# Optimization experiments

Measured on AMD Instinct MI355X. Metric: run time of the kernel, lower is better.

Reference implementation:

```python
import jax, jax.numpy as jnp
import numpy as np

B, T, F, M = 32, 256, 512, 4   # batch, pred_len (=d_model=state_size), feature_dim (=mamba seq), time-mark feats
N = F - M                      # number of variates in x_enc
T2 = 2 * T
EPS = 1e-5


def setup_inputs() -> dict:
    key = jax.random.key(0)
    it = iter(jax.random.split(key, 32))
    def nrm(*s):
        return jax.random.normal(next(it), s, jnp.float32) * 0.02
    inp = {
        "x_enc": jax.random.normal(next(it), (B, T, N), jnp.float32),
        "x_mark_enc": jax.random.normal(next(it), (B, T, M), jnp.float32),
        "x_dec": jnp.zeros((1, 1, 1), jnp.float32),
        "x_mark_dec": jnp.zeros((1, 1, 1), jnp.float32),
        # 3 structurally identical MambaBlocks -> stack params on leading dim 3
        "norm_w": jnp.ones((3, T), jnp.float32),
        "inp_W": nrm(3, T, T2), "inp_b": jnp.zeros((3, T2), jnp.float32),
        "conv_W": nrm(3, F, F, 3), "conv_b": jnp.zeros((3, F), jnp.float32),
        "convlin_W": nrm(3, T2, T2), "convlin_b": jnp.zeros((3, T2), jnp.float32),
        "fc1_W": nrm(3, T2, T2), "fc1_b": jnp.zeros((3, T2), jnp.float32),
        "fc2_W": nrm(3, T2, T), "fc2_b": jnp.zeros((3, T), jnp.float32),
        "fc3_W": nrm(3, T2, T), "fc3_b": jnp.zeros((3, T), jnp.float32),
        "D_W": nrm(3, T, T2), "D_b": jnp.zeros((3, T2), jnp.float32),
        "out_W": nrm(3, T2, T), "out_b": jnp.ones((3, T), jnp.float32),  # out_proj.bias init to 1.0
        "proj_W": nrm(T, T), "proj_b": jnp.zeros((T,), jnp.float32),
    }
    return inp


def _rmsnorm(x, w):
    return x * jax.lax.rsqrt(jnp.mean(x * x, -1, keepdims=True) + EPS) * w


def _conv1d(x, W, b):
    # x: [B, C, L], W: [C_out, C_in, 3], padding=1
    y = jax.lax.conv_general_dilated(x, W, (1,), [(1, 1)], dimension_numbers=("NCH", "OIH", "NCH"))
    return y + b[None, :, None]


def _s6(x, fc1W, fc1b, fc2W, fc2b, fc3W, fc3b):
    # h is zero-initialized each call, so dA=exp(delta*A) multiplies zeros and
    # y = einsum('bln,bldn->bld', C, x[...,None]*dB) = delta * x * <C,B>_n
    Bmat = x @ fc2W + fc2b                         # [B, L, n]
    Cmat = x @ fc3W + fc3b                         # [B, L, n]
    delta = jax.nn.softplus(x @ fc1W + fc1b)       # [B, L, d]
    cb = jnp.einsum("bln,bln->bl", Cmat, Bmat)   # contraction over state dim
    return delta * x * cb[:, :, None]


def _block(x, i, p):
    xn = _rmsnorm(x, p["norm_w"][i])
    xp = xn @ p["inp_W"][i] + p["inp_b"][i]                      # [B, F, 2T]
    xc = jax.nn.silu(_conv1d(xp, p["conv_W"][i], p["conv_b"][i]))
    xco = xc @ p["convlin_W"][i] + p["convlin_b"][i]
    xssm = _s6(xco, p["fc1_W"][i], p["fc1_b"][i], p["fc2_W"][i], p["fc2_b"][i], p["fc3_W"][i], p["fc3_b"][i])
    xres = jax.nn.silu(xn @ p["D_W"][i] + p["D_b"][i])
    return (jax.nn.silu(xssm) * xres) @ p["out_W"][i] + p["out_b"][i]


def _forward(x_enc, x_mark_enc, p):
    means = jax.lax.stop_gradient(jnp.mean(x_enc, 1, keepdims=True))  # detached in torch
    xe = x_enc - means
    stdev = jnp.sqrt(jnp.var(xe, axis=1, keepdims=True) + 1e-5)       # NOT detached in torch
    xe = xe / stdev
    x = jnp.concatenate([xe, x_mark_enc], axis=2).transpose(0, 2, 1)  # [B, F, T]
    for i in range(3):
        x = _block(x, i, p)
    dec = (x @ p["proj_W"] + p["proj_b"]).transpose(0, 2, 1)          # [B, T, F]
    return dec[:, :, :N] * stdev + means                              # pred_len == T


def reference(x_enc, x_mark_enc, x_dec, x_mark_dec, norm_w, inp_W, inp_b, conv_W, conv_b, convlin_W, convlin_b, fc1_W, fc1_b, fc2_W, fc2_b, fc3_W, fc3_b, D_W, D_b, out_W, out_b, proj_W, proj_b):
    p = dict(norm_w=norm_w, inp_W=inp_W, inp_b=inp_b, conv_W=conv_W, conv_b=conv_b, convlin_W=convlin_W, convlin_b=convlin_b, fc1_W=fc1_W, fc1_b=fc1_b, fc2_W=fc2_W, fc2_b=fc2_b, fc3_W=fc3_W, fc3_b=fc3_b, D_W=D_W, D_b=D_b, out_W=out_W, out_b=out_b, proj_W=proj_W, proj_b=proj_b)
    return _forward(x_enc, x_mark_enc, p)
```

## Files before the change

### kernel.cpp

```cpp
#include <hip/hip_runtime.h>
#include <hip/hip_bf16.h>
#include <math.h>

typedef __hip_bfloat16 bf16;
typedef short short8 __attribute__((ext_vector_type(8)));
typedef short short4v __attribute__((ext_vector_type(4)));
typedef float floatx4 __attribute__((ext_vector_type(4)));

constexpr int CB_ = 32;
constexpr int CT = 256;
constexpr int CF = 512;
constexpr int CN = 508;
constexpr int CM = 4;
constexpr int CT2 = 512;
constexpr int MROWS = CB_ * CF;
constexpr int PADL = 528;

__device__ __forceinline__ float b2f(bf16 v) { return __bfloat162float(v); }
__device__ __forceinline__ bf16 f2b(float v) { return __float2bfloat16(v); }
__device__ __forceinline__ short f2s(float v) {
    bf16 t = __float2bfloat16(v);
    return __builtin_bit_cast(short, t);
}
__device__ __forceinline__ float silu_f(float x) { return x / (1.0f + __expf(-x)); }
__device__ __forceinline__ float softplus_f(float x) {
    return fmaxf(x, 0.0f) + __logf(1.0f + __expf(-fabsf(x)));
}

__device__ __forceinline__ void gl_lds16(const bf16* g, short* l) {
    __builtin_amdgcn_global_load_lds(
        (const __attribute__((address_space(1))) unsigned int*)(g),
        (__attribute__((address_space(3))) unsigned int*)(l), 16, 0, 0);
}


constexpr int CONVN = 3 * 3 * 512 * 512;
constexpr int MTILES = 3520;
struct P8 { const float* s[8]; bf16* d[8]; };
__global__ __launch_bounds__(256) void prepack_all_kernel(P8 p, const float* __restrict__ nw,
                                                          const float* __restrict__ convW,
                                                          bf16* __restrict__ convD,
                                                          bf16* __restrict__ xpT,
                                                          float* __restrict__ CBv) {
    int bid = blockIdx.x;
    if (bid >= MTILES) {
        int idx = (bid - MTILES) * 256 + threadIdx.x;
        if (idx < CONVN) {
            int ci = idx & 511;
            int co = (idx >> 9) & 511;
            int it = idx >> 18;
            int tap = it % 3, ib = it / 3;
            convD[idx] = f2b(convW[(((size_t)(ib * 512 + co)) * 512 + ci) * 3 + tap]);
        } else if (idx < CONVN + 32768) {
            int j = idx - CONVN;
            int ci = j & 511;
            int w = (j >> 9) & 1;
            int b = j >> 10;
            xpT[((size_t)b * PADL + (w ? 513 : 0)) * 512 + ci] = f2b(0.0f);
        } else if (idx < CONVN + 32768 + MROWS) {
            CBv[idx - CONVN - 32768] = 0.0f;
        }
        return;
    }
    const int Ks[8]   = {256, 256, 512, 512, 512, 512, 512, 256};
    const int Ns[8]   = {512, 512, 512, 256, 256, 512, 256, 256};
    const int zs[8]   = {3, 3, 3, 3, 3, 3, 3, 1};
    const int dstr[8] = {262144, 262144, 524288, 524288, 524288, 262144, 131072, 65536};
    const int rml[8]  = {1, 1, 1, 2, 2, 1, 1, 1};
    const int rad[8]  = {0, 0, 0, 0, 1, 0, 0, 0};
    int m = 0, acc = 0;
    for (m = 0; m < 8; m++) {
        int c = (Ns[m] >> 5) * (Ks[m] >> 5) * zs[m];
        if (bid < acc + c) break;
        acc += c;
    }
    int lid = bid - acc;
    int K = Ks[m], N = Ns[m];
    int tx = N >> 5, ty = K >> 5;
    int z = lid / (tx * ty), rem = lid % (tx * ty);
    int k0 = (rem / tx) * 32, n0 = (rem % tx) * 32;
    const float* s = p.s[m] + (size_t)z * K * N;
    bf16* d = p.d[m] + (size_t)z * dstr[m];
    int mul = rml[m], add = rad[m];
    bool fold = (m <= 1);
    __shared__ float Ts[32][33];
    for (int e = threadIdx.x; e < 1024; e += 256) {
        int r = e >> 5, c = e & 31;
        float v = s[(size_t)(k0 + r) * N + n0 + c];
        if (fold) v *= nw[z * 256 + k0 + r];
        Ts[r][c] = v;
    }
    __syncthreads();
    for (int e = threadIdx.x; e < 1024; e += 256) {
        int r = e >> 5, c = e & 31;
        d[(size_t)((n0 + r) * mul + add) * K + k0 + c] = f2b(Ts[c][r]);
    }
}

__global__ __launch_bounds__(256) void buildx_kernel(
    const float* __restrict__ xe, const float* __restrict__ xm,
    float* __restrict__ means, float* __restrict__ stdev,
    bf16* __restrict__ X0, float* __restrict__ SCL) {
    __shared__ float L[256][65];
    __shared__ float red_s[4][64], red_q[4][64];
    __shared__ float stat_m[64], stat_i[64];
    int blk = blockIdx.x;
    int b = blk >> 3, f0 = (blk & 7) * 64;
    int tid = threadIdx.x;
    int j = tid & 63, tq = tid >> 6;
    int f = f0 + j;
    float ps = 0.f, pq = 0.f;
    const float* xep = xe + (size_t)b * CT * CN + f;
    const float* xmp = xm + (size_t)b * CT * CM + (f - CN);
    #pragma unroll 4
    for (int tt = 0; tt < 64; tt++) {
        int t = tq * 64 + tt;
        float v = (f < CN) ? xep[(size_t)t * CN] : xmp[(size_t)t * CM];
        L[t][j] = v;
        ps += v;
        pq += v * v;
    }
    red_s[tq][j] = ps;
    red_q[tq][j] = pq;
    __syncthreads();
    if (tid < 64) {
        int ff = f0 + tid;
        float s = red_s[0][tid] + red_s[1][tid] + red_s[2][tid] + red_s[3][tid];
        float q = red_q[0][tid] + red_q[1][tid] + red_q[2][tid] + red_q[3][tid];
        float mean, isd, msq;
        if (ff < CN) {
            mean = s * (1.0f / 256.0f);
            float var = fmaxf(q * (1.0f / 256.0f) - mean * mean, 0.0f);
            float sd = sqrtf(var + 1e-5f);
            isd = 1.0f / sd;
            means[b * CN + ff] = mean;
            stdev[b * CN + ff] = sd;
            msq = var / (var + 1e-5f);
        } else {
            mean = 0.0f;
            isd = 1.0f;
            msq = q * (1.0f / 256.0f);
        }
        stat_m[tid] = mean;
        stat_i[tid] = isd;
        SCL[b * 512 + ff] = rsqrtf(msq + 1e-5f);
    }
    __syncthreads();
    bf16* outp = X0 + ((size_t)(b * 512 + f0)) * 256;
    int t = tid;
    #pragma unroll 4
    for (int fp = 0; fp < 64; fp++) {
        float val = (L[t][fp] - stat_m[fp]) * stat_i[fp];
        outp[(size_t)fp * 256 + t] = f2b(val);
    }
}

template <int MODE>
__global__ __launch_bounds__(256) void mgemm_kernel(const bf16* __restrict__ A,
                                                    const bf16* __restrict__ Wt,
                                                    const float* __restrict__ b1,
                                                    const float* __restrict__ b2,
                                                    const float* __restrict__ SCL,
                                                    bf16* __restrict__ o1,
                                                    bf16* __restrict__ o2,
                                                    int K, int Ncols) {
    __shared__ __align__(16) short As[128 * 64];
    __shared__ __align__(16) short Bs[128 * 64];
    const int tid = threadIdx.x;
    const int lane = tid & 63;
    const int wave = tid >> 6;
    const int m0 = blockIdx.x * 128, n0 = blockIdx.y * 128;

    const int srow0 = wave * 32;
    const int lrow8 = lane >> 3;
    const int lcolS = (((lane & 7) ^ lrow8) << 3);

    const bf16* aPc[4];
    const bf16* bPc[4];
    short* aLc[4];
    short* bLc[4];
    #pragma unroll
    for (int c = 0; c < 4; c++) {
        aPc[c] = A + (size_t)(m0 + srow0 + c * 8 + lrow8) * K + lcolS;
        bPc[c] = Wt + (size_t)(n0 + srow0 + c * 8 + lrow8) * K + lcolS;
        aLc[c] = &As[(srow0 + c * 8) * 64];
        bLc[c] = &Bs[(srow0 + c * 8) * 64];
    }

    const int wm = (wave & 1) * 64, wn = (wave >> 1) * 64;
    const int fr = lane & 15, quad = lane >> 4;
    const int fr7 = fr & 7;

    floatx4 acc[4][4];
    #pragma unroll
    for (int i = 0; i < 4; i++)
        #pragma unroll
        for (int j = 0; j < 4; j++) acc[i][j] = (floatx4){0.f, 0.f, 0.f, 0.f};

    for (int k0 = 0; k0 < K; k0 += 64) {
        #pragma unroll
        for (int c = 0; c < 4; c++) {
            gl_lds16(aPc[c] + k0, aLc[c]);
            gl_lds16(bPc[c] + k0, bLc[c]);
        }
        __syncthreads();
        #pragma unroll
        for (int s = 0; s < 2; s++) {
            const int co = (((s * 4 + quad) ^ fr7) << 3);
            short8 af[4], bfv[4];
            #pragma unroll
            for (int i = 0; i < 4; i++) af[i] = *(const short8*)&As[(wm + i * 16 + fr) * 64 + co];
            #pragma unroll
            for (int j = 0; j < 4; j++) bfv[j] = *(const short8*)&Bs[(wn + j * 16 + fr) * 64 + co];
            #pragma unroll
            for (int i = 0; i < 4; i++)
                #pragma unroll
                for (int j = 0; j < 4; j++)
                    acc[i][j] = __builtin_amdgcn_mfma_f32_16x16x32_bf16(af[i], bfv[j], acc[i][j], 0, 0, 0);
        }
        __syncthreads();
    }

    if (MODE == 0) {
        #pragma unroll
        for (int j = 0; j < 4; j++) {
            int n = n0 + wn + j * 16 + fr;
            float bv = b1[n];
            #pragma unroll
            for (int i = 0; i < 4; i++) {
                int mb = m0 + wm + i * 16 + quad * 4;
                #pragma unroll
                for (int r = 0; r < 4; r++)
                    o1[(size_t)(mb + r) * Ncols + n] = f2b(acc[i][j][r] + bv);
            }
        }
    } else {
        if (n0 + wn < 512) {
            int b = (m0 + wm) >> 9;
            #pragma unroll
            for (int i = 0; i < 4; i++) {
                int mb = m0 + wm + i * 16 + quad * 4;
                float sclr[4];
                #pragma unroll
                for (int r = 0; r < 4; r++) sclr[r] = SCL[mb + r];
                #pragma unroll
                for (int j = 0; j < 4; j++) {
                    int n = n0 + wn + j * 16 + fr;
                    float bv = b1[n];
                    bf16* dst = o1 + ((size_t)b * PADL + n + 1) * 512;
                    int ci = mb & 511;
                    short4v pk;
                    #pragma unroll
                    for (int r = 0; r < 4; r++) pk[r] = f2s(acc[i][j][r] * sclr[r] + bv);
                    *(short4v*)(dst + ci) = pk;
                }
            }
        } else {
            #pragma unroll
            for (int i = 0; i < 4; i++) {
                int mb = m0 + wm + i * 16 + quad * 4;
                float sclr[4];
                #pragma unroll
                for (int r = 0; r < 4; r++) sclr[r] = SCL[mb + r];
                #pragma unroll
                for (int j = 0; j < 4; j++) {
                    int n = n0 + wn + j * 16 + fr;
                    float bv = b2[n - 512];
                    #pragma unroll
                    for (int r = 0; r < 4; r++)
                        o2[(size_t)(mb + r) * 512 + (n - 512)] =
                            f2b(silu_f(acc[i][j][r] * sclr[r] + bv));
                }
            }
        }
    }
}

template <int EPI>
__global__ __launch_bounds__(256) void g64_kernel(const bf16* __restrict__ A,
                                                  const bf16* __restrict__ Wt,
                                                  int K,
                                                  const float* __restrict__ b1,
                                                  const float* __restrict__ b2,
                                                  const float* __restrict__ CBin,
                                                  const bf16* __restrict__ Xres,
                                                  float* __restrict__ CBout,
                                                  bf16* __restrict__ o1,
                                                  int Ncols,
                                                  const float* __restrict__ means,
                                                  const float* __restrict__ stdev,
                                                  float* __restrict__ outf) {
    __shared__ __align__(16) short As[128 * 64];
    __shared__ __align__(16) short Bs[64 * 64];
    const int tid = threadIdx.x;
    const int lane = tid & 63;
    const int wave = tid >> 6;
    const int m0 = blockIdx.x * 128, n0 = blockIdx.y * 64;

    const int lrow8 = lane >> 3;
    const int lcolS = (((lane & 7) ^ lrow8) << 3);
    const int wm = (wave & 1) * 64, wn = (wave >> 1) * 32;
    const int fr = lane & 15, quad = lane >> 4;
    const int fr7 = fr & 7;

    floatx4 acc[4][2];
    #pragma unroll
    for (int i = 0; i < 4; i++)
        #pragma unroll
        for (int j = 0; j < 2; j++) acc[i][j] = (floatx4){0.f, 0.f, 0.f, 0.f};

    for (int k0 = 0; k0 < K; k0 += 64) {
        for (int ca = wave; ca < 16; ca += 4)
            gl_lds16(A + (size_t)(m0 + ca * 8 + lrow8) * K + k0 + lcolS, &As[ca * 512]);
        for (int cb = wave; cb < 8; cb += 4)
            gl_lds16(Wt + (size_t)(n0 + cb * 8 + lrow8) * K + k0 + lcolS, &Bs[cb * 512]);
        __syncthreads();
        #pragma unroll
        for (int s = 0; s < 2; s++) {
            const int co = (((s * 4 + quad) ^ fr7) << 3);
            short8 af[4], bfv[2];
            #pragma unroll
            for (int i = 0; i < 4; i++) af[i] = *(const short8*)&As[(wm + i * 16 + fr) * 64 + co];
            #pragma unroll
            for (int j = 0; j < 2; j++) bfv[j] = *(const short8*)&Bs[(wn + j * 16 + fr) * 64 + co];
            #pragma unroll
            for (int i = 0; i < 4; i++)
                #pragma unroll
                for (int j = 0; j < 2; j++)
                    acc[i][j] = __builtin_amdgcn_mfma_f32_16x16x32_bf16(af[i], bfv[j], acc[i][j], 0, 0, 0);
        }
        __syncthreads();
    }

    if (EPI == 0) {
        #pragma unroll
        for (int j = 0; j < 2; j++) {
            int n = n0 + wn + j * 16 + fr;
            float bv = b1[n];
            #pragma unroll
            for (int i = 0; i < 4; i++) {
                int mb = m0 + wm + i * 16 + quad * 4;
                #pragma unroll
                for (int r = 0; r < 4; r++)
                    o1[(size_t)(mb + r) * Ncols + n] = f2b(acc[i][j][r] + bv);
            }
        }
    } else if (EPI == 1) {
        float bv[2];
        #pragma unroll
        for (int j = 0; j < 2; j++) {
            int nn = n0 + wn + j * 16 + fr;
            int c = nn >> 1;
            bv[j] = (fr & 1) ? b2[c] : b1[c];
        }
        #pragma unroll
        for (int i = 0; i < 4; i++) {
            #pragma unroll
            for (int r = 0; r < 4; r++) {
                float s = 0.f;
                #pragma unroll
                for (int j = 0; j < 2; j++) {
                    float v = acc[i][j][r] + bv[j];
                    s += v * __shfl_xor(v, 1);
                }
                s += __shfl_xor(s, 2);
                s += __shfl_xor(s, 4);
                s += __shfl_xor(s, 8);
                if (fr == 0)
                    atomicAdd(&CBout[m0 + wm + i * 16 + quad * 4 + r], s * 0.5f);
            }
        }
    } else if (EPI == 2) {
        #pragma unroll
        for (int i = 0; i < 4; i++) {
            int mb = m0 + wm + i * 16 + quad * 4;
            float cbr[4];
            #pragma unroll
            for (int r = 0; r < 4; r++) cbr[r] = CBin[mb + r];
            #pragma unroll
            for (int j = 0; j < 2; j++) {
                int n = n0 + wn + j * 16 + fr;
                float bv = b1[n];
                #pragma unroll
                for (int r = 0; r < 4; r++) {
                    size_t off = (size_t)(mb + r) * 512 + n;
                    float delta = softplus_f(acc[i][j][r] + bv);
                    float xssm = delta * b2f(A[off]) * cbr[r];
                    o1[off] = f2b(silu_f(xssm) * b2f(Xres[off]));
                }
            }
        }
    } else {
        #pragma unroll
        for (int j = 0; j < 2; j++) {
            int t = n0 + wn + j * 16 + fr;
            float bv = b1[t];
            #pragma unroll
            for (int i = 0; i < 4; i++) {
                int mb = m0 + wm + i * 16 + quad * 4;
                int b = mb >> 9;
                int nv = mb & 511;
                if (nv < CN) {
                    floatx4 o;
                    #pragma unroll
                    for (int r = 0; r < 4; r++) {
                        int sn = b * CN + nv + r;
                        o[r] = (acc[i][j][r] + bv) * stdev[sn] + means[sn];
                    }
                    *(floatx4*)(outf + ((size_t)(b * CT + t)) * CN + nv) = o;
                }
            }
        }
    }
}

__global__ __launch_bounds__(256) void conv_mfma_kernel(const bf16* __restrict__ Wc,
                                                        const bf16* __restrict__ xpT,
                                                        const float* __restrict__ bias,
                                                        bf16* __restrict__ Out,
                                                        float* __restrict__ CBvZ) {
    __shared__ __align__(16) short As[3 * 64 * 64];
    __shared__ __align__(16) short Bs[72 * 64];
    const int tid = threadIdx.x;
    const int lane = tid & 63;
    const int wave = tid >> 6;
    int bx = blockIdx.x;
    if (bx < 128 && tid < 128) CBvZ[bx * 128 + tid] = 0.0f;
    int b = bx >> 6, rem = bx & 63;
    int mt = rem >> 3, nt = rem & 7;
    const int m0 = mt * 64, n0 = nt * 64;
    const bf16* xb = xpT + (size_t)b * PADL * 512;

    const int lrow8 = lane >> 3;
    const int lcolS = (((lane & 7) ^ lrow8) << 3);
    const int wm = (wave & 1) * 32, wn = (wave >> 1) * 32;
    const int fr = lane & 15, quad = lane >> 4;
    const int fr7 = fr & 7;

    floatx4 acc[2][2];
    #pragma unroll
    for (int i = 0; i < 2; i++)
        #pragma unroll
        for (int j = 0; j < 2; j++) acc[i][j] = (floatx4){0.f, 0.f, 0.f, 0.f};

    for (int k0 = 0; k0 < 512; k0 += 64) {
        for (int ga = wave; ga < 24; ga += 4) {
            int tap = ga >> 3, rg = ga & 7;
            gl_lds16(Wc + (size_t)tap * 262144 + (size_t)(m0 + rg * 8 + lrow8) * 512 + k0 + lcolS,
                     &As[tap * 4096 + rg * 512]);
        }
        for (int gb = wave; gb < 9; gb += 4) {
            gl_lds16(xb + (size_t)(n0 + gb * 8 + lrow8) * 512 + k0 + lcolS, &Bs[gb * 512]);
        }
        __syncthreads();
        #pragma unroll
        for (int s = 0; s < 2; s++) {
            const int sq = s * 4 + quad;
            #pragma unroll
            for (int tap = 0; tap < 3; tap++) {
                const int coA = ((sq ^ fr7) << 3);
                const int coB = ((sq ^ ((fr + tap) & 7)) << 3);
                short8 af[2], bfv[2];
                #pragma unroll
                for (int i = 0; i < 2; i++)
                    af[i] = *(const short8*)&As[tap * 4096 + (wm + i * 16 + fr) * 64 + coA];
                #pragma unroll
                for (int j = 0; j < 2; j++)
                    bfv[j] = *(const short8*)&Bs[(wn + j * 16 + fr + tap) * 64 + coB];
                #pragma unroll
                for (int i = 0; i < 2; i++)
                    #pragma unroll
                    for (int j = 0; j < 2; j++)
                        acc[i][j] = __builtin_amdgcn_mfma_f32_16x16x32_bf16(af[i], bfv[j], acc[i][j], 0, 0, 0);
            }
        }
        __syncthreads();
    }
    bf16* ob = Out + (size_t)b * CF * CT2;
    #pragma unroll
    for (int i = 0; i < 2; i++) {
        int mb = m0 + wm + i * 16 + quad * 4;
        #pragma unroll
        for (int r = 0; r < 4; r++) {
            float bv = bias[mb + r];
            #pragma unroll
            for (int j = 0; j < 2; j++) {
                int n = n0 + wn + j * 16 + fr;
                ob[(size_t)(mb + r) * CT2 + n] = f2b(silu_f(acc[i][j][r] + bv));
            }
        }
    }
}

__global__ __launch_bounds__(256) void gemm_scl_kernel(const bf16* __restrict__ A,
                                                       const bf16* __restrict__ Wt,
                                                       const float* __restrict__ bias,
                                                       bf16* __restrict__ Xo,
                                                       float* __restrict__ SCL) {
    __shared__ __align__(16) short As[32 * 64];
    __shared__ __align__(16) short Bs[256 * 64];
    __shared__ float red[4][32];
    const int tid = threadIdx.x;
    const int lane = tid & 63;
    const int wave = tid >> 6;
    const int m0 = blockIdx.x * 32;

    const int lrow8 = lane >> 3;
    const int lcolS = (((lane & 7) ^ lrow8) << 3);
    const int wn = wave * 64;
    const int fr = lane & 15, quad = lane >> 4;
    const int fr7 = fr & 7;

    floatx4 acc[2][4];
    #pragma unroll
    for (int i = 0; i < 2; i++)
        #pragma unroll
        for (int j = 0; j < 4; j++) acc[i][j] = (floatx4){0.f, 0.f, 0.f, 0.f};

    for (int k0 = 0; k0 < 512; k0 += 64) {
        for (int c = wave; c < 4; c += 4)
            gl_lds16(A + (size_t)(m0 + c * 8 + lrow8) * 512 + k0 + lcolS, &As[c * 512]);
        for (int c = wave; c < 32; c += 4)
            gl_lds16(Wt + (size_t)(c * 8 + lrow8) * 512 + k0 + lcolS, &Bs[c * 512]);
        __syncthreads();
        #pragma unroll
        for (int s = 0; s < 2; s++) {
            const int co = (((s * 4 + quad) ^ fr7) << 3);
            short8 af[2], bfv[4];
            #pragma unroll
            for (int i = 0; i < 2; i++) af[i] = *(const short8*)&As[(i * 16 + fr) * 64 + co];
            #pragma unroll
            for (int j = 0; j < 4; j++) bfv[j] = *(const short8*)&Bs[(wn + j * 16 + fr) * 64 + co];
            #pragma unroll
            for (int i = 0; i < 2; i++)
                #pragma unroll
                for (int j = 0; j < 4; j++)
                    acc[i][j] = __builtin_amdgcn_mfma_f32_16x16x32_bf16(af[i], bfv[j], acc[i][j], 0, 0, 0);
        }
        __syncthreads();
    }
    #pragma unroll
    for (int j = 0; j < 4; j++) {
        float bv = bias[wn + j * 16 + fr];
        #pragma unroll
        for (int i = 0; i < 2; i++)
            #pragma unroll
            for (int r = 0; r < 4; r++) acc[i][j][r] += bv;
    }
    #pragma unroll
    for (int i = 0; i < 2; i++) {
        #pragma unroll
        for (int r = 0; r < 4; r++) {
            float s = 0.f;
            #pragma unroll
            for (int j = 0; j < 4; j++) s += acc[i][j][r] * acc[i][j][r];
            #pragma unroll
            for (int o = 8; o > 0; o >>= 1) s += __shfl_xor(s, o);
            if (fr == 0) red[wave][i * 16 + quad * 4 + r] = s;
        }
    }
    __syncthreads();
    if (tid < 32) {
        float tot = red[0][tid] + red[1][tid] + red[2][tid] + red[3][tid];
        SCL[m0 + tid] = rsqrtf(tot * (1.0f / CT) + 1e-5f);
    }
    #pragma unroll
    for (int j = 0; j < 4; j++) {
        int n = wn + j * 16 + fr;
        #pragma unroll
        for (int i = 0; i < 2; i++) {
            int rl = i * 16 + quad * 4;
            #pragma unroll
            for (int r = 0; r < 4; r++)
                Xo[(size_t)(m0 + rl + r) * CT + n] = f2b(acc[i][j][r]);
        }
    }
}

extern "C" void kernel_launch(void* const* d_in, const int* in_sizes, int n_in,
                              void* d_out, int out_size, void* d_ws, size_t ws_size,
                              hipStream_t stream) {
    const float* x_enc  = (const float*)d_in[0];
    const float* x_mark = (const float*)d_in[1];
    const float* norm_w = (const float*)d_in[4];
    const float* inp_W  = (const float*)d_in[5];
    const float* inp_b  = (const float*)d_in[6];
    const float* conv_W = (const float*)d_in[7];
    const float* conv_b = (const float*)d_in[8];
    const float* convlin_W = (const float*)d_in[9];
    const float* convlin_b = (const float*)d_in[10];
    const float* fc1_W = (const float*)d_in[11];
    const float* fc1_b = (const float*)d_in[12];
    const float* fc2_W = (const float*)d_in[13];
    const float* fc2_b = (const float*)d_in[14];
    const float* fc3_W = (const float*)d_in[15];
    const float* fc3_b = (const float*)d_in[16];
    const float* D_W   = (const float*)d_in[17];
    const float* D_b   = (const float*)d_in[18];
    const float* out_W = (const float*)d_in[19];
    const float* out_b = (const float*)d_in[20];
    const float* proj_W = (const float*)d_in[21];
    const float* proj_b = (const float*)d_in[22];

    char* ws = (char*)d_ws;
    float* MEANS = (float*)(ws);
    float* STDEV = (float*)(ws + 65536);
    float* CBv   = (float*)(ws + 131072);
    float* SCL   = (float*)(ws + 196608);
    bf16* wt = (bf16*)(ws + 262144);
    bf16* wt_g1      = wt;
    bf16* wt_g3      = wt + 786432;
    bf16* wt_convlin = wt + 2359296;
    bf16* wt_out     = wt + 3145728;
    bf16* wt_proj    = wt + 3538944;
    bf16* wt_conv    = wt + 3604480;
    bf16* xpT = (bf16*)(ws + 12189696);
    const size_t POOLB = 16777216;
    bf16* pool[4] = {
        (bf16*)(ws + 29491200),
        (bf16*)(ws + 29491200 + POOLB),
        (bf16*)(ws + 29491200 + 2 * POOLB),
        (bf16*)(ws + 29491200 + 3 * POOLB),
    };
    float* out = (float*)d_out;

    P8 p;
    p.s[0] = inp_W;  p.d[0] = wt_g1;
    p.s[1] = D_W;    p.d[1] = wt_g1 + 131072;
    p.s[2] = fc1_W;  p.d[2] = wt_g3;
    p.s[3] = fc2_W;  p.d[3] = wt_g3 + 262144;
    p.s[4] = fc3_W;  p.d[4] = wt_g3 + 262144;
    p.s[5] = convlin_W; p.d[5] = wt_convlin;
    p.s[6] = out_W;  p.d[6] = wt_out;
    p.s[7] = proj_W; p.d[7] = wt_proj;
    int convBlocks = (CONVN + 32768 + MROWS + 255) / 256;
    prepack_all_kernel<<<MTILES + convBlocks, 256, 0, stream>>>(
        p, norm_w, conv_W, wt_conv, xpT, CBv);

    buildx_kernel<<<256, 256, 0, stream>>>(x_enc, x_mark, MEANS, STDEV, pool[0], SCL);

    int ia = 0, ico = 1, ires = 2, iout = 3;
    for (int i = 0; i < 3; i++) {
        bf16* A  = pool[ia];
        bf16* XCO = pool[ico];
        bf16* XRES = pool[ires];
        bf16* OUTP = pool[iout];

        mgemm_kernel<1><<<dim3(128, 8), 256, 0, stream>>>(
            A, wt_g1 + (size_t)i * 262144, inp_b + i * CT2, D_b + i * CT2, SCL,
            xpT, XRES, 256, 1024);
        conv_mfma_kernel<<<2048, 256, 0, stream>>>(wt_conv + (size_t)i * 786432, xpT,
                                                   conv_b + i * CF, A, CBv);
        g64_kernel<0><<<dim3(128, 8), 256, 0, stream>>>(
            A, wt_convlin + (size_t)i * 262144, 512, convlin_b + i * CT2, nullptr,
            nullptr, nullptr, nullptr, XCO, 512, nullptr, nullptr, nullptr);
        g64_kernel<1><<<dim3(128, 8), 256, 0, stream>>>(
            XCO, wt_g3 + (size_t)i * 524288 + 262144, 512, fc2_b + i * CT, fc3_b + i * CT,
            nullptr, nullptr, CBv, nullptr, 0, nullptr, nullptr, nullptr);
        g64_kernel<2><<<dim3(128, 8), 256, 0, stream>>>(
            XCO, wt_g3 + (size_t)i * 524288, 512, fc1_b + i * CT2, nullptr,
            CBv, XRES, nullptr, A, 512, nullptr, nullptr, nullptr);
        gemm_scl_kernel<<<512, 256, 0, stream>>>(
            A, wt_out + (size_t)i * 131072, out_b + i * CT, OUTP, SCL);

        int na = iout, nco = ia, nres = ico, nout = ires;
        ia = na; ico = nco; ires = nres; iout = nout;
    }

    g64_kernel<3><<<dim3(128, 4), 256, 0, stream>>>(
        pool[ia], wt_proj, 256, proj_b, nullptr, nullptr, nullptr, nullptr,
        nullptr, 0, MEANS, STDEV, out);
}
```

Measured before the change: 528.2 us.

## Double-buffer LDS in all GEMM kernels and fold input projection into g64

Adds a two-stage LDS ping-pong to the g64, conv and gemm_scl kernels, so the global-to-LDS load of the next K tile is issued before the current tile's MFMA work. This removes one barrier per K step and hides load latency. The 128x128 mgemm kernel is replaced by g64 with a new epilogue mode on a 128x64 tile grid. The conv weight prepack now reads three contiguous taps per thread instead of striding. The extra LDS doubles shared-memory use per block, which may lower occupancy, and the smaller input-projection tile reduces data reuse.

```diff
diff --git a/kernel.cpp b/kernel.cpp
--- a/kernel.cpp
+++ b/kernel.cpp
@@ -34,7 +34,7 @@
 }
 
 
-constexpr int CONVN = 3 * 3 * 512 * 512;
+constexpr int CONV3 = 3 * 512 * 512;
 constexpr int MTILES = 3520;
 struct P8 { const float* s[8]; bf16* d[8]; };
 __global__ __launch_bounds__(256) void prepack_all_kernel(P8 p, const float* __restrict__ nw,
@@ -45,20 +45,22 @@
     int bid = blockIdx.x;
     if (bid >= MTILES) {
         int idx = (bid - MTILES) * 256 + threadIdx.x;
-        if (idx < CONVN) {
+        if (idx < CONV3) {
             int ci = idx & 511;
             int co = (idx >> 9) & 511;
-            int it = idx >> 18;
-            int tap = it % 3, ib = it / 3;
-            convD[idx] = f2b(convW[(((size_t)(ib * 512 + co)) * 512 + ci) * 3 + tap]);
-        } else if (idx < CONVN + 32768) {
-            int j = idx - CONVN;
+            int ib = idx >> 18;
+            const float* src = convW + ((size_t)(ib * 512 + co) * 512 + ci) * 3;
+            #pragma unroll
+            for (int t = 0; t < 3; t++)
+                convD[(((size_t)(ib * 3 + t) * 512 + co) << 9) + ci] = f2b(src[t]);
+        } else if (idx < CONV3 + 32768) {
+            int j = idx - CONV3;
             int ci = j & 511;
             int w = (j >> 9) & 1;
             int b = j >> 10;
             xpT[((size_t)b * PADL + (w ? 513 : 0)) * 512 + ci] = f2b(0.0f);
-        } else if (idx < CONVN + 32768 + MROWS) {
-            CBv[idx - CONVN - 32768] = 0.0f;
+        } else if (idx < CONV3 + 32768 + MROWS) {
+            CBv[idx - CONV3 - 32768] = 0.0f;
         }
         return;
     }
@@ -155,143 +157,24 @@
     }
 }
 
-template <int MODE>
-__global__ __launch_bounds__(256) void mgemm_kernel(const bf16* __restrict__ A,
-                                                    const bf16* __restrict__ Wt,
-                                                    const float* __restrict__ b1,
-                                                    const float* __restrict__ b2,
-                                                    const float* __restrict__ SCL,
-                                                    bf16* __restrict__ o1,
-                                                    bf16* __restrict__ o2,
-                                                    int K, int Ncols) {
-    __shared__ __align__(16) short As[128 * 64];
-    __shared__ __align__(16) short Bs[128 * 64];
-    const int tid = threadIdx.x;
-    const int lane = tid & 63;
-    const int wave = tid >> 6;
-    const int m0 = blockIdx.x * 128, n0 = blockIdx.y * 128;
-
-    const int srow0 = wave * 32;
-    const int lrow8 = lane >> 3;
-    const int lcolS = (((lane & 7) ^ lrow8) << 3);
-
-    const bf16* aPc[4];
-    const bf16* bPc[4];
-    short* aLc[4];
-    short* bLc[4];
-    #pragma unroll
-    for (int c = 0; c < 4; c++) {
-        aPc[c] = A + (size_t)(m0 + srow0 + c * 8 + lrow8) * K + lcolS;
-        bPc[c] = Wt + (size_t)(n0 + srow0 + c * 8 + lrow8) * K + lcolS;
-        aLc[c] = &As[(srow0 + c * 8) * 64];
-        bLc[c] = &Bs[(srow0 + c * 8) * 64];
-    }
-
-    const int wm = (wave & 1) * 64, wn = (wave >> 1) * 64;
-    const int fr = lane & 15, quad = lane >> 4;
-    const int fr7 = fr & 7;
-
-    floatx4 acc[4][4];
-    #pragma unroll
-    for (int i = 0; i < 4; i++)
-        #pragma unroll
-        for (int j = 0; j < 4; j++) acc[i][j] = (floatx4){0.f, 0.f, 0.f, 0.f};
-
-    for (int k0 = 0; k0 < K; k0 += 64) {
-        #pragma unroll
-        for (int c = 0; c < 4; c++) {
-            gl_lds16(aPc[c] + k0, aLc[c]);
-            gl_lds16(bPc[c] + k0, bLc[c]);
-        }
-        __syncthreads();
-        #pragma unroll
-        for (int s = 0; s < 2; s++) {
-            const int co = (((s * 4 + quad) ^ fr7) << 3);
-            short8 af[4], bfv[4];
-            #pragma unroll
-            for (int i = 0; i < 4; i++) af[i] = *(const short8*)&As[(wm + i * 16 + fr) * 64 + co];
-            #pragma unroll
-            for (int j = 0; j < 4; j++) bfv[j] = *(const short8*)&Bs[(wn + j * 16 + fr) * 64 + co];
-            #pragma unroll
-            for (int i = 0; i < 4; i++)
-                #pragma unroll
-                for (int j = 0; j < 4; j++)
-                    acc[i][j] = __builtin_amdgcn_mfma_f32_16x16x32_bf16(af[i], bfv[j], acc[i][j], 0, 0, 0);
-        }
-        __syncthreads();
-    }
-
-    if (MODE == 0) {
-        #pragma unroll
-        for (int j = 0; j < 4; j++) {
-            int n = n0 + wn + j * 16 + fr;
-            float bv = b1[n];
-            #pragma unroll
-            for (int i = 0; i < 4; i++) {
-                int mb = m0 + wm + i * 16 + quad * 4;
-                #pragma unroll
-                for (int r = 0; r < 4; r++)
-                    o1[(size_t)(mb + r) * Ncols + n] = f2b(acc[i][j][r] + bv);
-            }
-        }
-    } else {
-        if (n0 + wn < 512) {
-            int b = (m0 + wm) >> 9;
-            #pragma unroll
-            for (int i = 0; i < 4; i++) {
-                int mb = m0 + wm + i * 16 + quad * 4;
-                float sclr[4];
-                #pragma unroll
-                for (int r = 0; r < 4; r++) sclr[r] = SCL[mb + r];
-                #pragma unroll
-                for (int j = 0; j < 4; j++) {
-                    int n = n0 + wn + j * 16 + fr;
-                    float bv = b1[n];
-                    bf16* dst = o1 + ((size_t)b * PADL + n + 1) * 512;
-                    int ci = mb & 511;
-                    short4v pk;
-                    #pragma unroll
-                    for (int r = 0; r < 4; r++) pk[r] = f2s(acc[i][j][r] * sclr[r] + bv);
-                    *(short4v*)(dst + ci) = pk;
-                }
-            }
-        } else {
-            #pragma unroll
-            for (int i = 0; i < 4; i++) {
-                int mb = m0 + wm + i * 16 + quad * 4;
-                float sclr[4];
-                #pragma unroll
-                for (int r = 0; r < 4; r++) sclr[r] = SCL[mb + r];
-                #pragma unroll
-                for (int j = 0; j < 4; j++) {
-                    int n = n0 + wn + j * 16 + fr;
-                    float bv = b2[n - 512];
-                    #pragma unroll
-                    for (int r = 0; r < 4; r++)
-                        o2[(size_t)(mb + r) * 512 + (n - 512)] =
-                            f2b(silu_f(acc[i][j][r] * sclr[r] + bv));
-                }
-            }
-        }
-    }
-}
-
 template <int EPI>
 __global__ __launch_bounds__(256) void g64_kernel(const bf16* __restrict__ A,
                                                   const bf16* __restrict__ Wt,
                                                   int K,
                                                   const float* __restrict__ b1,
                                                   const float* __restrict__ b2,
+                                                  const float* __restrict__ SCL,
                                                   const float* __restrict__ CBin,
                                                   const bf16* __restrict__ Xres,
                                                   float* __restrict__ CBout,
                                                   bf16* __restrict__ o1,
+                                                  bf16* __restrict__ o2,
                                                   int Ncols,
                                                   const float* __restrict__ means,
                                                   const float* __restrict__ stdev,
                                                   float* __restrict__ outf) {
-    __shared__ __align__(16) short As[128 * 64];
-    __shared__ __align__(16) short Bs[64 * 64];
+    __shared__ __align__(16) short As[2][128 * 64];
+    __shared__ __align__(16) short Bs[2][64 * 64];
     const int tid = threadIdx.x;
     const int lane = tid & 63;
     const int wave = tid >> 6;
@@ -309,28 +192,39 @@
         #pragma unroll
         for (int j = 0; j < 2; j++) acc[i][j] = (floatx4){0.f, 0.f, 0.f, 0.f};
 
-    for (int k0 = 0; k0 < K; k0 += 64) {
+    auto STAGE = [&](int buf, int k0) {
         for (int ca = wave; ca < 16; ca += 4)
-            gl_lds16(A + (size_t)(m0 + ca * 8 + lrow8) * K + k0 + lcolS, &As[ca * 512]);
+            gl_lds16(A + (size_t)(m0 + ca * 8 + lrow8) * K + k0 + lcolS, &As[buf][ca * 512]);
         for (int cb = wave; cb < 8; cb += 4)
-            gl_lds16(Wt + (size_t)(n0 + cb * 8 + lrow8) * K + k0 + lcolS, &Bs[cb * 512]);
-        __syncthreads();
+            gl_lds16(Wt + (size_t)(n0 + cb * 8 + lrow8) * K + k0 + lcolS, &Bs[buf][cb * 512]);
+    };
+    auto COMPUTE = [&](int buf) {
         #pragma unroll
         for (int s = 0; s < 2; s++) {
             const int co = (((s * 4 + quad) ^ fr7) << 3);
             short8 af[4], bfv[2];
             #pragma unroll
-            for (int i = 0; i < 4; i++) af[i] = *(const short8*)&As[(wm + i * 16 + fr) * 64 + co];
-            #pragma unroll
-            for (int j = 0; j < 2; j++) bfv[j] = *(const short8*)&Bs[(wn + j * 16 + fr) * 64 + co];
+            for (int i = 0; i < 4; i++) af[i] = *(const short8*)&As[buf][(wm + i * 16 + fr) * 64 + co];
+            #pragma unroll
+            for (int j = 0; j < 2; j++) bfv[j] = *(const short8*)&Bs[buf][(wn + j * 16 + fr) * 64 + co];
             #pragma unroll
             for (int i = 0; i < 4; i++)
                 #pragma unroll
                 for (int j = 0; j < 2; j++)
                     acc[i][j] = __builtin_amdgcn_mfma_f32_16x16x32_bf16(af[i], bfv[j], acc[i][j], 0, 0, 0);
         }
+    };
+
+    STAGE(0, 0);
+    __syncthreads();
+    int cur = 0;
+    for (int k0 = 64; k0 < K; k0 += 64) {
+        STAGE(cur ^ 1, k0);
+        COMPUTE(cur);
         __syncthreads();
-    }
+        cur ^= 1;
+    }
+    COMPUTE(cur);
 
     if (EPI == 0) {
         #pragma unroll
@@ -390,7 +284,7 @@
                 }
             }
         }
-    } else {
+    } else if (EPI == 3) {
         #pragma unroll
         for (int j = 0; j < 2; j++) {
             int t = n0 + wn + j * 16 + fr;
@@ -411,6 +305,45 @@
                 }
             }
         }
+    } else {
+        if (n0 < 512) {
+            int b = (m0 + wm) >> 9;
+            #pragma unroll
+            for (int i = 0; i < 4; i++) {
+                int mb = m0 + wm + i * 16 + quad * 4;
+                float sclr[4];
+                #pragma unroll
+                for (int r = 0; r < 4; r++) sclr[r] = SCL[mb + r];
+                int ci = mb & 511;
+                #pragma unroll
+                for (int j = 0; j < 2; j++) {
+                    int n = n0 + wn + j * 16 + fr;
+                    float bv = b1[n];
+                    bf16* dst = o1 + ((size_t)b * PADL + n + 1) * 512;
+                    short4v pk;
+                    #pragma unroll
+                    for (int r = 0; r < 4; r++) pk[r] = f2s(acc[i][j][r] * sclr[r] + bv);
+                    *(short4v*)(dst + ci) = pk;
+                }
+            }
+        } else {
+            #pragma unroll
+            for (int i = 0; i < 4; i++) {
+                int mb = m0 + wm + i * 16 + quad * 4;
+                float sclr[4];
+                #pragma unroll
+                for (int r = 0; r < 4; r++) sclr[r] = SCL[mb + r];
+                #pragma unroll
+                for (int j = 0; j < 2; j++) {
+                    int n = n0 + wn + j * 16 + fr;
+                    float bv = b2[n - 512];
+                    #pragma unroll
+                    for (int r = 0; r < 4; r++)
+                        o2[(size_t)(mb + r) * 512 + (n - 512)] =
+                            f2b(silu_f(acc[i][j][r] * sclr[r] + bv));
+                }
+            }
+        }
     }
 }
 
@@ -419,8 +352,8 @@
                                                         const float* __restrict__ bias,
                                                         bf16* __restrict__ Out,
                                                         float* __restrict__ CBvZ) {
-    __shared__ __align__(16) short As[3 * 64 * 64];
-    __shared__ __align__(16) short Bs[72 * 64];
+    __shared__ __align__(16) short As[2][3 * 64 * 64];
+    __shared__ __align__(16) short Bs[2][72 * 64];
     const int tid = threadIdx.x;
     const int lane = tid & 63;
     const int wave = tid >> 6;
@@ -443,16 +376,17 @@
         #pragma unroll
         for (int j = 0; j < 2; j++) acc[i][j] = (floatx4){0.f, 0.f, 0.f, 0.f};
 
-    for (int k0 = 0; k0 < 512; k0 += 64) {
+    auto STAGE = [&](int buf, int k0) {
         for (int ga = wave; ga < 24; ga += 4) {
             int tap = ga >> 3, rg = ga & 7;
             gl_lds16(Wc + (size_t)tap * 262144 + (size_t)(m0 + rg * 8 + lrow8) * 512 + k0 + lcolS,
-                     &As[tap * 4096 + rg * 512]);
+                     &As[buf][tap * 4096 + rg * 512]);
         }
         for (int gb = wave; gb < 9; gb += 4) {
-            gl_lds16(xb + (size_t)(n0 + gb * 8 + lrow8) * 512 + k0 + lcolS, &Bs[gb * 512]);
-        }
-        __syncthreads();
+            gl_lds16(xb + (size_t)(n0 + gb * 8 + lrow8) * 512 + k0 + lcolS, &Bs[buf][gb * 512]);
+        }
+    };
+    auto COMPUTE = [&](int buf) {
         #pragma unroll
         for (int s = 0; s < 2; s++) {
             const int sq = s * 4 + quad;
@@ -463,10 +397,10 @@
                 short8 af[2], bfv[2];
                 #pragma unroll
                 for (int i = 0; i < 2; i++)
-                    af[i] = *(const short8*)&As[tap * 4096 + (wm + i * 16 + fr) * 64 + coA];
+                    af[i] = *(const short8*)&As[buf][tap * 4096 + (wm + i * 16 + fr) * 64 + coA];
                 #pragma unroll
                 for (int j = 0; j < 2; j++)
-                    bfv[j] = *(const short8*)&Bs[(wn + j * 16 + fr + tap) * 64 + coB];
+                    bfv[j] = *(const short8*)&Bs[buf][(wn + j * 16 + fr + tap) * 64 + coB];
                 #pragma unroll
                 for (int i = 0; i < 2; i++)
                     #pragma unroll
@@ -474,8 +408,19 @@
                         acc[i][j] = __builtin_amdgcn_mfma_f32_16x16x32_bf16(af[i], bfv[j], acc[i][j], 0, 0, 0);
             }
         }
+    };
+
+    STAGE(0, 0);
+    __syncthreads();
+    int cur = 0;
+    for (int k0 = 64; k0 < 512; k0 += 64) {
+        STAGE(cur ^ 1, k0);
+        COMPUTE(cur);
         __syncthreads();
-    }
+        cur ^= 1;
+    }
+    COMPUTE(cur);
+
     bf16* ob = Out + (size_t)b * CF * CT2;
     #pragma unroll
     for (int i = 0; i < 2; i++) {
@@ -497,8 +442,8 @@
                                                        const float* __restrict__ bias,
                                                        bf16* __restrict__ Xo,
                                                        float* __restrict__ SCL) {
-    __shared__ __align__(16) short As[32 * 64];
-    __shared__ __align__(16) short Bs[256 * 64];
+    __shared__ __align__(16) short As[2][32 * 64];
+    __shared__ __align__(16) short Bs[2][256 * 64];
     __shared__ float red[4][32];
     const int tid = threadIdx.x;
     const int lane = tid & 63;
@@ -517,28 +462,40 @@
         #pragma unroll
         for (int j = 0; j < 4; j++) acc[i][j] = (floatx4){0.f, 0.f, 0.f, 0.f};
 
-    for (int k0 = 0; k0 < 512; k0 += 64) {
+    auto STAGE = [&](int buf, int k0) {
         for (int c = wave; c < 4; c += 4)
-            gl_lds16(A + (size_t)(m0 + c * 8 + lrow8) * 512 + k0 + lcolS, &As[c * 512]);
+            gl_lds16(A + (size_t)(m0 + c * 8 + lrow8) * 512 + k0 + lcolS, &As[buf][c * 512]);
         for (int c = wave; c < 32; c += 4)
-            gl_lds16(Wt + (size_t)(c * 8 + lrow8) * 512 + k0 + lcolS, &Bs[c * 512]);
-        __syncthreads();
+            gl_lds16(Wt + (size_t)(c * 8 + lrow8) * 512 + k0 + lcolS, &Bs[buf][c * 512]);
+    };
+    auto COMPUTE = [&](int buf) {
         #pragma unroll
         for (int s = 0; s < 2; s++) {
             const int co = (((s * 4 + quad) ^ fr7) << 3);
             short8 af[2], bfv[4];
             #pragma unroll
-            for (int i = 0; i < 2; i++) af[i] = *(const short8*)&As[(i * 16 + fr) * 64 + co];
-            #pragma unroll
-            for (int j = 0; j < 4; j++) bfv[j] = *(const short8*)&Bs[(wn + j * 16 + fr) * 64 + co];
+            for (int i = 0; i < 2; i++) af[i] = *(const short8*)&As[buf][(i * 16 + fr) * 64 + co];
+            #pragma unroll
+            for (int j = 0; j < 4; j++) bfv[j] = *(const short8*)&Bs[buf][(wn + j * 16 + fr) * 64 + co];
             #pragma unroll
             for (int i = 0; i < 2; i++)
                 #pragma unroll
                 for (int j = 0; j < 4; j++)
                     acc[i][j] = __builtin_amdgcn_mfma_f32_16x16x32_bf16(af[i], bfv[j], acc[i][j], 0, 0, 0);
         }
+    };
+
+    STAGE(0, 0);
+    __syncthreads();
+    int cur = 0;
+    for (int k0 = 64; k0 < 512; k0 += 64) {
+        STAGE(cur ^ 1, k0);
+        COMPUTE(cur);
         __syncthreads();
-    }
+        cur ^= 1;
+    }
+    COMPUTE(cur);
+
     #pragma unroll
     for (int j = 0; j < 4; j++) {
         float bv = bias[wn + j * 16 + fr];
@@ -633,8 +590,8 @@
     p.s[5] = convlin_W; p.d[5] = wt_convlin;
     p.s[6] = out_W;  p.d[6] = wt_out;
     p.s[7] = proj_W; p.d[7] = wt_proj;
-    int convBlocks = (CONVN + 32768 + MROWS + 255) / 256;
-    prepack_all_kernel<<<MTILES + convBlocks, 256, 0, stream>>>(
+    int tailBlocks = (CONV3 + 32768 + MROWS + 255) / 256;
+    prepack_all_kernel<<<MTILES + tailBlocks, 256, 0, stream>>>(
         p, norm_w, conv_W, wt_conv, xpT, CBv);
 
     buildx_kernel<<<256, 256, 0, stream>>>(x_enc, x_mark, MEANS, STDEV, pool[0], SCL);
@@ -646,20 +603,20 @@
         bf16* XRES = pool[ires];
         bf16* OUTP = pool[iout];
 
-        mgemm_kernel<1><<<dim3(128, 8), 256, 0, stream>>>(
-            A, wt_g1 + (size_t)i * 262144, inp_b + i * CT2, D_b + i * CT2, SCL,
-            xpT, XRES, 256, 1024);
+        g64_kernel<4><<<dim3(128, 16), 256, 0, stream>>>(
+            A, wt_g1 + (size_t)i * 262144, 256, inp_b + i * CT2, D_b + i * CT2, SCL,
+            nullptr, nullptr, nullptr, xpT, XRES, 1024, nullptr, nullptr, nullptr);
         conv_mfma_kernel<<<2048, 256, 0, stream>>>(wt_conv + (size_t)i * 786432, xpT,
                                                    conv_b + i * CF, A, CBv);
         g64_kernel<0><<<dim3(128, 8), 256, 0, stream>>>(
-            A, wt_convlin + (size_t)i * 262144, 512, convlin_b + i * CT2, nullptr,
-            nullptr, nullptr, nullptr, XCO, 512, nullptr, nullptr, nullptr);
+            A, wt_convlin + (size_t)i * 262144, 512, convlin_b + i * CT2, nullptr, nullptr,
+            nullptr, nullptr, nullptr, XCO, nullptr, 512, nullptr, nullptr, nullptr);
         g64_kernel<1><<<dim3(128, 8), 256, 0, stream>>>(
             XCO, wt_g3 + (size_t)i * 524288 + 262144, 512, fc2_b + i * CT, fc3_b + i * CT,
-            nullptr, nullptr, CBv, nullptr, 0, nullptr, nullptr, nullptr);
+            nullptr, nullptr, nullptr, CBv, nullptr, nullptr, 0, nullptr, nullptr, nullptr);
         g64_kernel<2><<<dim3(128, 8), 256, 0, stream>>>(
-            XCO, wt_g3 + (size_t)i * 524288, 512, fc1_b + i * CT2, nullptr,
-            CBv, XRES, nullptr, A, 512, nullptr, nullptr, nullptr);
+            XCO, wt_g3 + (size_t)i * 524288, 512, fc1_b + i * CT2, nullptr, nullptr,
+            CBv, XRES, nullptr, A, nullptr, 512, nullptr, nullptr, nullptr);
         gemm_scl_kernel<<<512, 256, 0, stream>>>(
             A, wt_out + (size_t)i * 131072, out_b + i * CT, OUTP, SCL);
 
@@ -668,6 +625,6 @@
     }
 
     g64_kernel<3><<<dim3(128, 4), 256, 0, stream>>>(
-        pool[ia], wt_proj, 256, proj_b, nullptr, nullptr, nullptr, nullptr,
-        nullptr, 0, MEANS, STDEV, out);
-}
+        pool[ia], wt_proj, 256, proj_b, nullptr, nullptr, nullptr, nullptr, nullptr,
+        nullptr, nullptr, 0, MEANS, STDEV, out);
+}
```

After: 590.9 us. +11.9%, slower.
